# Kernel optimization log

Hardware: AMD Instinct MI355X
Metric: run time of the kernel (lower is better)

Reference implementation:

```python
import jax, jax.numpy as jnp
import numpy as np

N, K = 8192, 16          # nodes, neighbours per node
FEAT = 128               # size + 1 (attention input dim)
DIST = 128               # distance_size (query dim & block width)
H, D = 8, 128            # heads, per-head attention size
HID = 128                # MLP hidden size
SCALE = 1.0 / np.sqrt(D)


def _lin_init(k, i, o):
    return jax.random.normal(k, (i, o), jnp.float32) / np.sqrt(i)


def setup_inputs() -> dict:
    key = jax.random.key(0)
    ks = jax.random.split(key, 12)
    z = lambda n: jnp.zeros((n,), jnp.float32)
    return {
        "features": jax.random.normal(ks[0], (N, FEAT), jnp.float32),
        "distance_features": jax.random.normal(ks[1], (N, DIST), jnp.float32),
        "structure": jax.random.randint(ks[2], (N, K), 0, N, jnp.int32),
        # attention projections
        "Wq": _lin_init(ks[3], DIST, H * D), "bq": z(H * D),
        "Wk": _lin_init(ks[4], FEAT, H * D), "bk": z(H * D),
        "Wv": _lin_init(ks[5], FEAT, H * D), "bv": z(H * D),
        "Wo": _lin_init(ks[6], H * D, DIST), "bo": z(DIST),
        # local MLP: depth=3 hidden layers + output layer
        "W1": _lin_init(ks[7], DIST, HID), "b1": z(HID),
        "W2": _lin_init(ks[8], HID, HID), "b2": z(HID),
        "W3": _lin_init(ks[9], HID, HID), "b3": z(HID),
        "W4": _lin_init(ks[10], HID, DIST), "b4": z(DIST),
    }


def reference(features, distance_features, structure,
              Wq, bq, Wk, bk, Wv, bv, Wo, bo,
              W1, b1, W2, b2, W3, b3, W4, b4):
    # bn / local_bn are identity (batch_norm=False); dropout identity (eval)
    normed = distance_features

    # NeighbourDotMultiHeadAttention: queries from distance feats, K/V from node feats
    q = (normed @ Wq + bq).reshape(N, H, D)
    k = (features @ Wk + bk).reshape(N, H, D)
    v = (features @ Wv + bv).reshape(N, H, D)
    kg = k[structure]                                  # [N, K, H, D] neighbour keys
    vg = v[structure]                                  # [N, K, H, D] neighbour values
    logits = jnp.einsum('nhd,nkhd->nkh', q, kg) * SCALE
    attn = jax.nn.softmax(logits, axis=1)              # over K neighbours
    att = jnp.einsum('nkh,nkhd->nhd', attn, vg).reshape(N, H * D)
    att_out = att @ Wo + bo                            # [N, DIST]

    out = distance_features + att_out                  # residual 1

    # local MLP with relu activations
    h = jax.nn.relu(out @ W1 + b1)
    h = jax.nn.relu(h @ W2 + b2)
    h = jax.nn.relu(h @ W3 + b3)
    mlp = h @ W4 + b4

    return out + mlp                                   # residual 2
```

## Files before the change

kernel.cpp:

```cpp
#include <hip/hip_runtime.h>
#include <hip/hip_bf16.h>

typedef float f32x4 __attribute__((ext_vector_type(4)));
typedef short s16x8 __attribute__((ext_vector_type(8)));
typedef unsigned short u16;

#define N_NODES 8192
#define KNBR 16
#define SCALE 0.08838834764831845f

__device__ __forceinline__ float bf2f(u16 h) {
    unsigned v = ((unsigned)h) << 16;
    return __builtin_bit_cast(float, v);
}
__device__ __forceinline__ u16 f2bf(float f) {
    __hip_bfloat16 h = __float2bfloat16(f);
    return __builtin_bit_cast(u16, h);
}

__global__ void prep_kernel(const float* __restrict__ feat, const float* __restrict__ dist,
                            const float* __restrict__ Wq, const float* __restrict__ Wk,
                            const float* __restrict__ Wv, const float* __restrict__ Wo,
                            const float* __restrict__ W1, const float* __restrict__ W2,
                            const float* __restrict__ W3, const float* __restrict__ W4,
                            const float* __restrict__ bq, const float* __restrict__ bk,
                            const float* __restrict__ bv,
                            u16* __restrict__ featb, u16* __restrict__ distb,
                            u16* __restrict__ Wqkvt, u16* __restrict__ Wot,
                            u16* __restrict__ Wmlpt, float* __restrict__ bqkv) {
    int gid = blockIdx.x * 256 + threadIdx.x;
    featb[gid] = f2bf(feat[gid]);
    distb[gid] = f2bf(dist[gid]);
    if (gid < 3072 * 128) {
        int col = gid >> 7, k = gid & 127;
        float v = (col < 1024) ? Wq[k * 1024 + col]
                : (col < 2048) ? Wk[k * 1024 + (col - 1024)]
                               : Wv[k * 1024 + (col - 2048)];
        Wqkvt[gid] = f2bf(v);
    }
    if (gid < 128 * 1024) {
        int col = gid >> 10, k = gid & 1023;
        Wot[gid] = f2bf(Wo[k * 128 + col]);
    }
    if (gid < 4 * 128 * 128) {
        int m = gid >> 14, r = gid & 16383;
        int col = r >> 7, k = r & 127;
        const float* Wm = (m == 0) ? W1 : (m == 1) ? W2 : (m == 2) ? W3 : W4;
        Wmlpt[gid] = f2bf(Wm[k * 128 + col]);
    }
    if (gid < 3072) {
        bqkv[gid] = (gid < 1024) ? bq[gid] : (gid < 2048) ? bk[gid - 1024] : bv[gid - 2048];
    }
}

__global__ __launch_bounds__(256, 2) void qkv_gemm(const u16* __restrict__ featb,
                                                   const u16* __restrict__ distb,
                                                   const u16* __restrict__ Wqkvt,
                                                   const float* __restrict__ bqkv,
                                                   u16* __restrict__ qkvh) {
    const int rt = blockIdx.x, ct = blockIdx.y;
    const int w = threadIdx.x >> 6, l = threadIdx.x & 63;
    const int rbase = rt * 256 + w * 64;
    const int cbase = ct * 128;
    const u16* A = (ct < 8) ? distb : featb;

    s16x8 af[4][4];
#pragma unroll
    for (int mf = 0; mf < 4; mf++) {
        const u16* ar = A + (size_t)(rbase + mf * 16 + (l & 15)) * 128 + ((l >> 4) * 8);
#pragma unroll
        for (int kk = 0; kk < 4; kk++) af[mf][kk] = *(const s16x8*)(ar + kk * 32);
    }

    f32x4 acc[4][8];
#pragma unroll
    for (int mf = 0; mf < 4; mf++)
#pragma unroll
        for (int nf = 0; nf < 8; nf++) acc[mf][nf] = (f32x4){0.f, 0.f, 0.f, 0.f};

#pragma unroll
    for (int nf = 0; nf < 8; nf++) {
        const u16* bp = Wqkvt + (size_t)(cbase + nf * 16 + (l & 15)) * 128 + ((l >> 4) * 8);
        s16x8 b0 = *(const s16x8*)bp;
        s16x8 b1 = *(const s16x8*)(bp + 32);
        s16x8 b2 = *(const s16x8*)(bp + 64);
        s16x8 b3 = *(const s16x8*)(bp + 96);
#pragma unroll
        for (int mf = 0; mf < 4; mf++) {
            acc[mf][nf] = __builtin_amdgcn_mfma_f32_16x16x32_bf16(af[mf][0], b0, acc[mf][nf], 0, 0, 0);
            acc[mf][nf] = __builtin_amdgcn_mfma_f32_16x16x32_bf16(af[mf][1], b1, acc[mf][nf], 0, 0, 0);
            acc[mf][nf] = __builtin_amdgcn_mfma_f32_16x16x32_bf16(af[mf][2], b2, acc[mf][nf], 0, 0, 0);
            acc[mf][nf] = __builtin_amdgcn_mfma_f32_16x16x32_bf16(af[mf][3], b3, acc[mf][nf], 0, 0, 0);
        }
    }

    float bias[8];
#pragma unroll
    for (int nf = 0; nf < 8; nf++) bias[nf] = bqkv[cbase + nf * 16 + (l & 15)];

    u16* obase = qkvh + ((size_t)ct * 8192 + rbase) * 128 + (l & 15);
#pragma unroll
    for (int mf = 0; mf < 4; mf++) {
#pragma unroll
        for (int nf = 0; nf < 8; nf++) {
#pragma unroll
            for (int r = 0; r < 4; r++) {
                const int row = mf * 16 + (l >> 4) * 4 + r;
                obase[(size_t)row * 128 + nf * 16] = f2bf(acc[mf][nf][r] + bias[nf]);
            }
        }
    }
}

__global__ __launch_bounds__(256) void attn_kernel(const u16* __restrict__ qkvh,
                                                   const int* __restrict__ structure,
                                                   u16* __restrict__ attb) {
    const int head = blockIdx.x & 7, chunk = blockIdx.x >> 3;
    const int w = threadIdx.x >> 6, l = threadIdx.x & 63;
    const int ni = l >> 3, lh = l & 7;
    const int n = chunk * 32 + w * 8 + ni;

    const u16* qrow = qkvh + ((size_t)(0 * 8 + head) * 8192 + n) * 128 + lh * 16;
    float qf[16];
    {
        s16x8 q0 = *(const s16x8*)qrow;
        s16x8 q1 = *(const s16x8*)(qrow + 8);
#pragma unroll
        for (int t = 0; t < 8; t++) { qf[t] = bf2f((u16)q0[t]); qf[8 + t] = bf2f((u16)q1[t]); }
    }

    const int2 idx2 = ((const int2*)structure)[n * 8 + lh];

    const u16* kbase = qkvh + (size_t)(1 * 8 + head) * 8192 * 128;
    const u16* vbase = qkvh + (size_t)(2 * 8 + head) * 8192 * 128;

    float logit[16];
#pragma unroll
    for (int j = 0; j < 16; j++) {
        int idx = __shfl(j & 1 ? idx2.y : idx2.x, (ni << 3) | (j >> 1));
        const u16* krow = kbase + (size_t)idx * 128 + lh * 16;
        s16x8 k0 = *(const s16x8*)krow;
        s16x8 k1 = *(const s16x8*)(krow + 8);
        float s = 0.f;
#pragma unroll
        for (int t = 0; t < 8; t++) {
            s += qf[t] * bf2f((u16)k0[t]);
            s += qf[8 + t] * bf2f((u16)k1[t]);
        }
        s += __shfl_xor(s, 1);
        s += __shfl_xor(s, 2);
        s += __shfl_xor(s, 4);
        logit[j] = s * SCALE;
    }

    float m = logit[0];
#pragma unroll
    for (int j = 1; j < 16; j++) m = fmaxf(m, logit[j]);
    float sum = 0.f;
#pragma unroll
    for (int j = 0; j < 16; j++) { logit[j] = __expf(logit[j] - m); sum += logit[j]; }
    const float inv = 1.f / sum;

    float acc[16];
#pragma unroll
    for (int t = 0; t < 16; t++) acc[t] = 0.f;
#pragma unroll
    for (int j = 0; j < 16; j++) {
        int idx = __shfl(j & 1 ? idx2.y : idx2.x, (ni << 3) | (j >> 1));
        const u16* vrow = vbase + (size_t)idx * 128 + lh * 16;
        s16x8 v0 = *(const s16x8*)vrow;
        s16x8 v1 = *(const s16x8*)(vrow + 8);
        const float p = logit[j] * inv;
#pragma unroll
        for (int t = 0; t < 8; t++) {
            acc[t]     += p * bf2f((u16)v0[t]);
            acc[8 + t] += p * bf2f((u16)v1[t]);
        }
    }

    s16x8 o0, o1;
#pragma unroll
    for (int t = 0; t < 8; t++) { o0[t] = (short)f2bf(acc[t]); o1[t] = (short)f2bf(acc[8 + t]); }
    u16* orow = attb + (size_t)n * 1024 + head * 128 + lh * 16;
    *(s16x8*)orow = o0;
    *(s16x8*)(orow + 8) = o1;
}

__global__ __launch_bounds__(128) void out_mlp(const u16* __restrict__ attb,
                                               const u16* __restrict__ Wot,
                                               const u16* __restrict__ Wmlpt,
                                               const float* __restrict__ dist,
                                               const float* __restrict__ bo,
                                               const float* __restrict__ b1,
                                               const float* __restrict__ b2,
                                               const float* __restrict__ b3,
                                               const float* __restrict__ b4,
                                               float* __restrict__ out) {
    __shared__ __attribute__((aligned(16))) u16 act[2][16][136];
    const int w = threadIdx.x >> 6, l = threadIdx.x & 63;
    const int rbase = blockIdx.x * 16;
    const int cb = w * 64;

    f32x4 acc[4];
#pragma unroll
    for (int i = 0; i < 4; i++) acc[i] = (f32x4){0.f, 0.f, 0.f, 0.f};

    const u16* ap = attb + (size_t)(rbase + (l & 15)) * 1024 + ((l >> 4) * 8);
#pragma unroll 4
    for (int kk = 0; kk < 32; kk++) {
        s16x8 af = *(const s16x8*)(ap + kk * 32);
#pragma unroll
        for (int nf = 0; nf < 4; nf++) {
            const u16* bp = Wot + (size_t)(cb + nf * 16 + (l & 15)) * 1024 + kk * 32 + ((l >> 4) * 8);
            s16x8 bf = *(const s16x8*)bp;
            acc[nf] = __builtin_amdgcn_mfma_f32_16x16x32_bf16(af, bf, acc[nf], 0, 0, 0);
        }
    }

    float outsave[4][4];
#pragma unroll
    for (int nf = 0; nf < 4; nf++) {
        const int gcol = cb + nf * 16 + (l & 15);
        const float bv = bo[gcol];
#pragma unroll
        for (int r = 0; r < 4; r++) {
            const int rl = (l >> 4) * 4 + r;
            float v = acc[nf][r] + bv + dist[(size_t)(rbase + rl) * 128 + gcol];
            outsave[nf][r] = v;
            act[0][rl][gcol] = f2bf(v);
        }
    }
    __syncthreads();

#pragma unroll
    for (int layer = 0; layer < 4; layer++) {
        const int rd = layer & 1, wr = (layer + 1) & 1;
        f32x4 macc[4];
#pragma unroll
        for (int i = 0; i < 4; i++) macc[i] = (f32x4){0.f, 0.f, 0.f, 0.f};
#pragma unroll
        for (int kk = 0; kk < 4; kk++) {
            s16x8 af = *(const s16x8*)&act[rd][l & 15][kk * 32 + ((l >> 4) * 8)];
#pragma unroll
            for (int nf = 0; nf < 4; nf++) {
                const u16* bp = Wmlpt + layer * 16384
                              + (size_t)(cb + nf * 16 + (l & 15)) * 128 + kk * 32 + ((l >> 4) * 8);
                s16x8 bf = *(const s16x8*)bp;
                macc[nf] = __builtin_amdgcn_mfma_f32_16x16x32_bf16(af, bf, macc[nf], 0, 0, 0);
            }
        }
        const float* bias = (layer == 0) ? b1 : (layer == 1) ? b2 : (layer == 2) ? b3 : b4;
        if (layer < 3) {
#pragma unroll
            for (int nf = 0; nf < 4; nf++) {
                const int gcol = cb + nf * 16 + (l & 15);
                const float bv = bias[gcol];
#pragma unroll
                for (int r = 0; r < 4; r++) {
                    const int rl = (l >> 4) * 4 + r;
                    act[wr][rl][gcol] = f2bf(fmaxf(macc[nf][r] + bv, 0.f));
                }
            }
            __syncthreads();
        } else {
#pragma unroll
            for (int nf = 0; nf < 4; nf++) {
                const int gcol = cb + nf * 16 + (l & 15);
                const float bv = bias[gcol];
#pragma unroll
                for (int r = 0; r < 4; r++) {
                    const int rl = (l >> 4) * 4 + r;
                    out[(size_t)(rbase + rl) * 128 + gcol] = outsave[nf][r] + macc[nf][r] + bv;
                }
            }
        }
    }
}

extern "C" void kernel_launch(void* const* d_in, const int* in_sizes, int n_in,
                              void* d_out, int out_size, void* d_ws, size_t ws_size,
                              hipStream_t stream) {
    const float* features = (const float*)d_in[0];
    const float* dist     = (const float*)d_in[1];
    const int*   structure= (const int*)d_in[2];
    const float* Wq = (const float*)d_in[3];  const float* bq = (const float*)d_in[4];
    const float* Wk = (const float*)d_in[5];  const float* bk = (const float*)d_in[6];
    const float* Wv = (const float*)d_in[7];  const float* bv = (const float*)d_in[8];
    const float* Wo = (const float*)d_in[9];  const float* bo = (const float*)d_in[10];
    const float* W1 = (const float*)d_in[11]; const float* b1 = (const float*)d_in[12];
    const float* W2 = (const float*)d_in[13]; const float* b2 = (const float*)d_in[14];
    const float* W3 = (const float*)d_in[15]; const float* b3 = (const float*)d_in[16];
    const float* W4 = (const float*)d_in[17]; const float* b4 = (const float*)d_in[18];
    float* out = (float*)d_out;

    u16* wsp   = (u16*)d_ws;
    u16* qkvh  = wsp;
    u16* attb  = qkvh  + (size_t)3 * 8 * 8192 * 128;
    u16* featb = attb  + (size_t)8192 * 1024;
    u16* distb = featb + (size_t)8192 * 128;
    u16* Wqkvt = distb + (size_t)8192 * 128;
    u16* Wot   = Wqkvt + (size_t)3072 * 128;
    u16* Wmlpt = Wot   + (size_t)128 * 1024;
    float* bqkv = (float*)(Wmlpt + (size_t)4 * 128 * 128);

    prep_kernel<<<4096, 256, 0, stream>>>(features, dist, Wq, Wk, Wv, Wo, W1, W2, W3, W4,
                                          bq, bk, bv, featb, distb, Wqkvt, Wot, Wmlpt, bqkv);
    qkv_gemm<<<dim3(32, 24), 256, 0, stream>>>(featb, distb, Wqkvt, bqkv, qkvh);
    attn_kernel<<<2048, 256, 0, stream>>>(qkvh, structure, attb);
    out_mlp<<<512, 128, 0, stream>>>(attb, Wot, Wmlpt, dist, bo, b1, b2, b3, b4, out);
}
```

Before: 189.6 us.

## Store QKV in fp16 and use packed half math with batched gathers in attention

The QKV projection now writes fp16 instead of bf16. The attention kernel computes dot products and value accumulation with packed fp16 vector arithmetic instead of converting each element to fp32. Neighbour K/V rows are gathered in batches of eight before computing, so more memory loads are in flight at once. This reduces ALU conversion work and improves latency hiding. The cost is reduced precision: fp16 accumulation of logits and outputs, plus overflow risk. The output MLP loop unroll is also raised from 4 to 8.

New measurement: 189.4 us. About the same (-0.1%).

```diff
diff --git a/kernel.cpp b/kernel.cpp
--- a/kernel.cpp
+++ b/kernel.cpp
@@ -3,6 +3,9 @@
 
 typedef float f32x4 __attribute__((ext_vector_type(4)));
 typedef short s16x8 __attribute__((ext_vector_type(8)));
+typedef _Float16 h8v __attribute__((ext_vector_type(8)));
+typedef _Float16 h4v __attribute__((ext_vector_type(4)));
+typedef _Float16 h2v __attribute__((ext_vector_type(2)));
 typedef unsigned short u16;
 
 #define N_NODES 8192
@@ -15,6 +18,10 @@
 }
 __device__ __forceinline__ u16 f2bf(float f) {
     __hip_bfloat16 h = __float2bfloat16(f);
+    return __builtin_bit_cast(u16, h);
+}
+__device__ __forceinline__ u16 f2h(float f) {
+    _Float16 h = (_Float16)f;
     return __builtin_bit_cast(u16, h);
 }
 
@@ -106,7 +113,7 @@
 #pragma unroll
             for (int r = 0; r < 4; r++) {
                 const int row = mf * 16 + (l >> 4) * 4 + r;
-                obase[(size_t)row * 128 + nf * 16] = f2bf(acc[mf][nf][r] + bias[nf]);
+                obase[(size_t)row * 128 + nf * 16] = f2h(acc[mf][nf][r] + bias[nf]);
             }
         }
     }
@@ -120,37 +127,38 @@
     const int ni = l >> 3, lh = l & 7;
     const int n = chunk * 32 + w * 8 + ni;
 
-    const u16* qrow = qkvh + ((size_t)(0 * 8 + head) * 8192 + n) * 128 + lh * 16;
-    float qf[16];
-    {
-        s16x8 q0 = *(const s16x8*)qrow;
-        s16x8 q1 = *(const s16x8*)(qrow + 8);
-#pragma unroll
-        for (int t = 0; t < 8; t++) { qf[t] = bf2f((u16)q0[t]); qf[8 + t] = bf2f((u16)q1[t]); }
-    }
+    const _Float16* qtab = (const _Float16*)qkvh;
+    const _Float16* qrow = qtab + ((size_t)head * 8192 + n) * 128 + lh * 16;
+    h8v q0 = *(const h8v*)qrow;
+    h8v q1 = *(const h8v*)(qrow + 8);
 
     const int2 idx2 = ((const int2*)structure)[n * 8 + lh];
-
-    const u16* kbase = qkvh + (size_t)(1 * 8 + head) * 8192 * 128;
-    const u16* vbase = qkvh + (size_t)(2 * 8 + head) * 8192 * 128;
+    const _Float16* kbase = qtab + (size_t)(8 + head) * 8192 * 128;
+    const _Float16* vbase = qtab + (size_t)(16 + head) * 8192 * 128;
 
     float logit[16];
 #pragma unroll
-    for (int j = 0; j < 16; j++) {
-        int idx = __shfl(j & 1 ? idx2.y : idx2.x, (ni << 3) | (j >> 1));
-        const u16* krow = kbase + (size_t)idx * 128 + lh * 16;
-        s16x8 k0 = *(const s16x8*)krow;
-        s16x8 k1 = *(const s16x8*)(krow + 8);
-        float s = 0.f;
-#pragma unroll
-        for (int t = 0; t < 8; t++) {
-            s += qf[t] * bf2f((u16)k0[t]);
-            s += qf[8 + t] * bf2f((u16)k1[t]);
-        }
-        s += __shfl_xor(s, 1);
-        s += __shfl_xor(s, 2);
-        s += __shfl_xor(s, 4);
-        logit[j] = s * SCALE;
+    for (int half = 0; half < 2; half++) {
+        h8v kd0[8], kd1[8];
+#pragma unroll
+        for (int j8 = 0; j8 < 8; j8++) {
+            const int j = half * 8 + j8;
+            int idx = __shfl(j & 1 ? idx2.y : idx2.x, (ni << 3) | (j >> 1));
+            const _Float16* krow = kbase + (size_t)idx * 128 + lh * 16;
+            kd0[j8] = *(const h8v*)krow;
+            kd1[j8] = *(const h8v*)(krow + 8);
+        }
+#pragma unroll
+        for (int j8 = 0; j8 < 8; j8++) {
+            h8v a = kd0[j8] * q0 + kd1[j8] * q1;
+            h4v a4 = a.lo + a.hi;
+            h2v a2 = a4.lo + a4.hi;
+            float s = (float)a2.x + (float)a2.y;
+            s += __shfl_xor(s, 1);
+            s += __shfl_xor(s, 2);
+            s += __shfl_xor(s, 4);
+            logit[half * 8 + j8] = s * SCALE;
+        }
     }
 
     float m = logit[0];
@@ -161,26 +169,33 @@
     for (int j = 0; j < 16; j++) { logit[j] = __expf(logit[j] - m); sum += logit[j]; }
     const float inv = 1.f / sum;
 
-    float acc[16];
-#pragma unroll
-    for (int t = 0; t < 16; t++) acc[t] = 0.f;
-#pragma unroll
-    for (int j = 0; j < 16; j++) {
-        int idx = __shfl(j & 1 ? idx2.y : idx2.x, (ni << 3) | (j >> 1));
-        const u16* vrow = vbase + (size_t)idx * 128 + lh * 16;
-        s16x8 v0 = *(const s16x8*)vrow;
-        s16x8 v1 = *(const s16x8*)(vrow + 8);
-        const float p = logit[j] * inv;
-#pragma unroll
-        for (int t = 0; t < 8; t++) {
-            acc[t]     += p * bf2f((u16)v0[t]);
-            acc[8 + t] += p * bf2f((u16)v1[t]);
+    h8v acc0 = (h8v)((_Float16)0.f);
+    h8v acc1 = (h8v)((_Float16)0.f);
+#pragma unroll
+    for (int half = 0; half < 2; half++) {
+        h8v vd0[8], vd1[8];
+#pragma unroll
+        for (int j8 = 0; j8 < 8; j8++) {
+            const int j = half * 8 + j8;
+            int idx = __shfl(j & 1 ? idx2.y : idx2.x, (ni << 3) | (j >> 1));
+            const _Float16* vrow = vbase + (size_t)idx * 128 + lh * 16;
+            vd0[j8] = *(const h8v*)vrow;
+            vd1[j8] = *(const h8v*)(vrow + 8);
+        }
+#pragma unroll
+        for (int j8 = 0; j8 < 8; j8++) {
+            const _Float16 p = (_Float16)(logit[half * 8 + j8] * inv);
+            acc0 += vd0[j8] * p;
+            acc1 += vd1[j8] * p;
         }
     }
 
     s16x8 o0, o1;
 #pragma unroll
-    for (int t = 0; t < 8; t++) { o0[t] = (short)f2bf(acc[t]); o1[t] = (short)f2bf(acc[8 + t]); }
+    for (int t = 0; t < 8; t++) {
+        o0[t] = (short)f2bf((float)acc0[t]);
+        o1[t] = (short)f2bf((float)acc1[t]);
+    }
     u16* orow = attb + (size_t)n * 1024 + head * 128 + lh * 16;
     *(s16x8*)orow = o0;
     *(s16x8*)(orow + 8) = o1;
@@ -206,7 +221,7 @@
     for (int i = 0; i < 4; i++) acc[i] = (f32x4){0.f, 0.f, 0.f, 0.f};
 
     const u16* ap = attb + (size_t)(rbase + (l & 15)) * 1024 + ((l >> 4) * 8);
-#pragma unroll 4
+#pragma unroll 8
     for (int kk = 0; kk < 32; kk++) {
         s16x8 af = *(const s16x8*)(ap + kk * 32);
 #pragma unroll
```
